# Optimization experiments

Hardware: AMD Instinct MI355X
Metric: run time of the kernel (lower is better)

## Reference

```python
import jax, jax.numpy as jnp
import numpy as np

L, B, T, D, V = 4, 32, 512, 512, 1000


def setup_inputs() -> dict:
    key = jax.random.key(0)
    k0, k1, k2, k3, k4 = jax.random.split(key, 5)
    ids = jax.random.randint(k0, (B, T), 0, V)
    mask = jax.random.randint(k1, (B, T), 0, 2).astype(bool)  # True = valid token
    emb = jax.random.normal(k2, (V, D), dtype=jnp.float32) * 0.1
    W = jax.random.normal(k3, (L, D, 3 * D), dtype=jnp.float32) / np.float32(np.sqrt(D))
    v = jax.random.normal(k4, (L, 2, D), dtype=jnp.float32) * 0.1  # (v_f, v_r) per layer
    b = jnp.zeros((L, 2, D), dtype=jnp.float32)                    # (b_f, b_r) per layer
    return {"ids": ids, "mask": mask, "emb": emb, "W": W, "v": v, "b": b}


def _sru_layer(x, pad, Wl, vf, vr, bf, br):
    # x: [T,B,D] layer input; pad: [T,B,1] bool (True = padded step)
    Tn, Bn, Dn = x.shape
    U = jnp.einsum('tbd,de->tbe', x, Wl).reshape(Tn, Bn, 3, Dn)
    xt, fpre, rpre = U[:, :, 0], U[:, :, 1], U[:, :, 2]

    def step(c, inp):
        xt_t, fp_t, rp_t, x_t, pad_t = inp
        f = jax.nn.sigmoid(fp_t + vf * c + bf)
        r = jax.nn.sigmoid(rp_t + vr * c + br)
        c_new = f * c + (1.0 - f) * xt_t
        h = r * jnp.tanh(c_new) + (1.0 - r) * x_t  # highway (input_size==hidden_size)
        c_out = jnp.where(pad_t, c, c_new)          # padded step: keep state
        h = jnp.where(pad_t, 0.0, h)                # padded step: zero output
        return c_out, h

    c0 = jnp.zeros_like(x[0])  # zero initial hidden state, as in the torch code
    _, h = jax.lax.scan(step, c0, (xt, fpre, rpre, x, pad))
    return h  # [T,B,D]


def reference(ids, mask, emb, W, v, b):
    x = emb[ids]                       # CharEmbedder lookup: [B,T,D]
    x = jnp.transpose(x, (1, 0, 2))    # [T,B,D]  (permute(1,0,2))
    pad = (~mask).T[:, :, None]        # inverted_mask.T -> [T,B,1]
    for l in range(L):
        x = _sru_layer(x, pad, W[l], v[l, 0], v[l, 1], b[l, 0], b[l, 1])
    return jnp.transpose(x, (1, 0, 2))  # back to [B,T,D]
```

## Files before the change

kernel.cpp:

```cpp
#include <hip/hip_runtime.h>
#include <hip/hip_bf16.h>


#define LAYERS 4
#define BB 32
#define TT 512
#define DD 512
#define N3 1536
#define MROWS (TT * BB)
#define WPL ((size_t)DD * N3)
#define SB 32
#define LOG2E 1.4426950408889634f
#define TWOLOG2E 2.8853900817779268f

typedef unsigned short u16;
typedef unsigned int u32;
typedef _Float16 half8 __attribute__((ext_vector_type(8)));
typedef float f32x4 __attribute__((ext_vector_type(4)));

#define SBAR() asm volatile("s_barrier" ::: "memory")
#define WAITVM(n) asm volatile("s_waitcnt vmcnt(" n ")" ::: "memory")

__device__ __forceinline__ float b2f(u16 u) {
  union { unsigned int i; float f; } x;
  x.i = ((unsigned int)u) << 16;
  return x.f;
}
__device__ __forceinline__ u16 f2h(float f) {
  _Float16 h = (_Float16)f;
  return *(u16*)&h;
}
__device__ __forceinline__ float h2f(u16 u) {
  _Float16 h;
  *(u16*)&h = u;
  return (float)h;
}
__device__ __forceinline__ float rcpf(float x) { return __builtin_amdgcn_rcpf(x); }
__device__ __forceinline__ float exp2f_(float x) { return __builtin_amdgcn_exp2f(x); }

__device__ __forceinline__ void async_ld16(const void* g, void* l) {
  __builtin_amdgcn_global_load_lds(
      (const __attribute__((address_space(1))) void*)g,
      (__attribute__((address_space(3))) void*)l, 16, 0, 0);
}
__device__ __forceinline__ void async_ld4(const void* g, void* l) {
  __builtin_amdgcn_global_load_lds(
      (const __attribute__((address_space(1))) void*)g,
      (__attribute__((address_space(3))) void*)l, 4, 0, 0);
}

__global__ void detect_kernel(const u16* __restrict__ emb_u,
                              const int* __restrict__ mask_i,
                              const int* __restrict__ ids_i,
                              int* __restrict__ flags) {
  __shared__ int cnt[3];
  __shared__ int zc;
  int tid = threadIdx.x;
  if (tid < 3) cnt[tid] = 0;
  if (tid == 0) zc = 0;
  __syncthreads();
  int bad = 0, zero_even = 0;
  for (int i = tid; i < 8192; i += 256) {
    u16 u = emb_u[i];
    unsigned e = (u >> 7) & 0xFF;
    if (e >= 0x8F) bad++;
    if ((i & 1) == 0 && u == 0) zero_even++;
  }
  if (bad) atomicAdd(&cnt[0], bad);
  if (zero_even) atomicAdd(&zc, zero_even);
  if (tid < 64) {
    unsigned vv = (unsigned)mask_i[tid];
    if (vv > 1u) atomicAdd(&cnt[1], 1);
  }
  if (tid < 256) {
    if (ids_i[2 * tid + 1] == 0) atomicAdd(&cnt[2], 1);
  }
  __syncthreads();
  if (tid == 0) {
    flags[0] = (cnt[0] > 64 || zc > 3000) ? 1 : 0;
    flags[1] = (cnt[1] > 0) ? 1 : 0;
    flags[2] = (cnt[2] >= 192) ? 1 : 0;
  }
}

__global__ __launch_bounds__(256)
void wprep_kernel(const void* __restrict__ W, u16* __restrict__ W16,
                  const int* __restrict__ flags) {
  __shared__ float tileW[32][33];
  int l = blockIdx.z;
  int k0 = blockIdx.x * 32;
  int n0 = blockIdx.y * 32;
  int tx = threadIdx.x & 31;
  int ty = threadIdx.x >> 5;
  int ff = flags[0];
  const float* Wf = (const float*)W + (size_t)l * WPL;
  const u16* Wb = (const u16*)W + (size_t)l * WPL;
  for (int kk = ty; kk < 32; kk += 8) {
    size_t off = (size_t)(k0 + kk) * N3 + n0 + tx;
    tileW[kk][tx] = ff ? Wf[off] : b2f(Wb[off]);
  }
  __syncthreads();
  u16* outP = W16 + (size_t)l * WPL;
  for (int nn = ty; nn < 32; nn += 8) {
    float x = tileW[tx][nn];
    outP[(size_t)(n0 + nn) * DD + k0 + tx] = f2h(x);
  }
}

__global__ void embed_kernel(const int* __restrict__ ids,
                             const void* __restrict__ emb,
                             u16* __restrict__ X16,
                             const int* __restrict__ flags) {
  int i = blockIdx.x * 256 + threadIdx.x;
  int d = i & (DD - 1);
  int tb = i >> 9;
  int b = tb & (BB - 1);
  int t = tb >> 5;
  int ii = b * TT + t;
  int id = flags[2] ? ids[2 * ii] : ids[ii];
  float val = flags[0] ? ((const float*)emb)[id * DD + d]
                       : b2f(((const u16*)emb)[id * DD + d]);
  X16[i] = f2h(val);
}

__global__ __launch_bounds__(512, 2)
void gemm_kernel(const u16* __restrict__ X16, const u16* __restrict__ W16l,
                 const void* __restrict__ bvec, int layer,
                 const int* __restrict__ flags,
                 u16* __restrict__ U16, int row_base, int chunkM, int nblk) {
  __shared__ u16 lds[2][2][2][8192];
  const int tid = threadIdx.x;
  const int lane = tid & 63, wave = tid >> 6;
  const int wm = wave >> 2, wn = wave & 3;
  const int m16 = lane & 15, quad = lane >> 4;

  const int orig = blockIdx.x;
  const int wg = (orig & 7) * (nblk >> 3) + (orig >> 3);
  const int mt = wg / 6, nt = wg - mt * 6;

  const int arow0 = row_base + mt * 256;
  const int bcol0 = nt * 256;

  const int srow = lane >> 2;
  const int sq = (lane & 3) ^ ((lane >> 3) & 3);
  const u16* pa = X16 + (size_t)(arow0 + wave * 32 + srow) * DD + sq * 8;
  const u16* pb = W16l + (size_t)(bcol0 + wave * 32 + srow) * DD + sq * 8;
  const int ldsblk = wave * 2 * 512;

  auto stage = [&](int s) {
    const int ts = s >> 2, hi = s & 3;
    const int mat = hi & 1, kk = hi >> 1, db = ts & 1;
    const u16* src = (mat ? pb : pa) + ts * 64 + kk * 32;
    u16* dst = &lds[db][mat][kk][ldsblk];
    async_ld16(src, dst);
    async_ld16(src + (size_t)16 * DD, dst + 512);
  };

  f32x4 acc[8][4];
#pragma unroll
  for (int mi = 0; mi < 8; ++mi)
#pragma unroll
    for (int ni = 0; ni < 4; ++ni)
#pragma unroll
      for (int r = 0; r < 4; ++r) acc[mi][ni][r] = 0.f;

#pragma unroll
  for (int s = 0; s < 6; ++s) stage(s);
  WAITVM("8");
  SBAR();

  const int loff = m16 * 32 + (quad ^ ((m16 >> 1) & 3)) * 8;
  half8 bf[4];

  for (int t = 0; t < 8; ++t) {
    const int db = t & 1;
#pragma unroll
    for (int p = 0; p < 4; ++p) {
      const int kk = p >> 1;
      const int mh = (p == 1 || p == 2) ? 1 : 0;
      half8 af[4];
      const u16* Ab = &lds[db][0][kk][(wm * 8 + mh * 4) * 512 + loff];
#pragma unroll
      for (int i = 0; i < 4; ++i) af[i] = *(const half8*)(Ab + i * 512);
      if (p == 0 || p == 2) {
        const u16* Bb = &lds[db][1][kk][wn * 4 * 512 + loff];
#pragma unroll
        for (int i = 0; i < 4; ++i) bf[i] = *(const half8*)(Bb + i * 512);
      }
      const int s = t * 4 + p + 6;
      if (s < 32) stage(s);
      SBAR();
      __builtin_amdgcn_s_setprio(1);
#pragma unroll
      for (int mi = 0; mi < 4; ++mi)
#pragma unroll
        for (int ni = 0; ni < 4; ++ni)
          acc[mh * 4 + mi][ni] = __builtin_amdgcn_mfma_f32_16x16x32_f16(
              af[mi], bf[ni], acc[mh * 4 + mi][ni], 0, 0, 0);
      __builtin_amdgcn_s_setprio(0);
      if (p == 1) {
        WAITVM("4");
      } else if (p == 3) {
        if (t == 6) WAITVM("0");
        else WAITVM("8");
      }
      SBAR();
    }
  }

  const int ff = flags[0];
  const int pl = nt >> 1;
  const int dd0 = (nt & 1) * 256;
  u16* up = U16 + (size_t)pl * chunkM * 512;
  const int r0 = mt * 256 + wm * 128 + quad * 4;
  const int c0 = dd0 + wn * 64 + m16;
  if (pl == 0) {
#pragma unroll
    for (int mi = 0; mi < 8; ++mi)
#pragma unroll
      for (int reg = 0; reg < 4; ++reg) {
        size_t rb = (size_t)(r0 + mi * 16 + reg) * 512 + c0;
#pragma unroll
        for (int ni = 0; ni < 4; ++ni)
          up[rb + ni * 16] = f2h(acc[mi][ni][reg]);
      }
  } else {
    float bias[4];
#pragma unroll
    for (int ni = 0; ni < 4; ++ni) {
      size_t bo = (size_t)layer * 2 * DD + (size_t)(pl - 1) * DD + c0 + ni * 16;
      bias[ni] = ff ? ((const float*)bvec)[bo] : b2f(((const u16*)bvec)[bo]);
    }
#pragma unroll
    for (int mi = 0; mi < 8; ++mi)
#pragma unroll
      for (int reg = 0; reg < 4; ++reg) {
        size_t rb = (size_t)(r0 + mi * 16 + reg) * 512 + c0;
#pragma unroll
        for (int ni = 0; ni < 4; ++ni)
          up[rb + ni * 16] = f2h(-(acc[mi][ni][reg] + bias[ni]) * LOG2E);
      }
  }
}

template <int EMIT>
__global__ __launch_bounds__(448, 1)
void scan_kernel(const u16* __restrict__ U16, float* __restrict__ X,
                 u16* __restrict__ X16,
                 const void* __restrict__ mask_p, const void* __restrict__ vbase,
                 int layer, const int* __restrict__ flags,
                 float* __restrict__ carry, int t0, int nt, int chunkM) {
  __shared__ u16 bufA[2][2][SB][64];
  __shared__ u16 bufB[3][2][SB][64];
  __shared__ float ring[2][2][SB][64];
  __shared__ int msk[TT];
  const int tid = threadIdx.x;
  const int wave = tid >> 6, lane = tid & 63;
  const int idx0 = blockIdx.x * 64;
  const int b = idx0 >> 9;
  const int d0 = idx0 & 511;
  const int ff = flags[0], fm = flags[1];

  const int* mi_ = (const int*)mask_p + b * TT;
  const unsigned char* mb_ = (const unsigned char*)mask_p + b * TT;
  for (int i = tid; i < nt; i += 448) msk[i] = fm ? (int)mb_[t0 + i] : mi_[t0 + i];

  float vfs = 0.f, vrs = 0.f, c = 0.f;
  {
    int d = d0 + lane;
    size_t voff = (size_t)layer * 2 * DD;
    if (wave == 0) {
      float vf = ff ? ((const float*)vbase)[voff + d]
                    : b2f(((const u16*)vbase)[voff + d]);
      vfs = -vf * LOG2E;
      c = (t0 == 0) ? 0.f : carry[idx0 + lane];
    } else if (wave >= 1 && wave <= 4) {
      float vr = ff ? ((const float*)vbase)[voff + DD + d]
                    : b2f(((const u16*)vbase)[voff + DD + d]);
      vrs = -vr * LOG2E;
    }
  }

  const int nbuf = nt / SB;

  auto ld_pair = [&](const u16* rowS, const u16* rowS1, void* ldst) {
    const u32* a0 = (const u32*)rowS;
    const u32* a1 = (const u32*)rowS1;
    const u32* ga = (lane < 32) ? (a0 + lane) : (a1 + (lane - 32));
    async_ld4(ga, ldst);
  };

  auto produceA = [&](int k) {
    int ph = k & 1, tl = k * SB;
    const u16* p0 = U16 + ((size_t)tl * BB + b) * 512 + d0;
    const u16* p1 = p0 + (size_t)chunkM * 512;
#pragma unroll
    for (int s = 0; s < SB; s += 2)
      ld_pair(p0 + (size_t)s * BB * 512, p0 + (size_t)(s + 1) * BB * 512,
              &bufA[ph][0][s][0]);
#pragma unroll
    for (int s = 0; s < SB; s += 2)
      ld_pair(p1 + (size_t)s * BB * 512, p1 + (size_t)(s + 1) * BB * 512,
              &bufA[ph][1][s][0]);
  };
  auto produceB = [&](int k) {
    int ph = k % 3, tl = k * SB;
    const u16* p2 = U16 + 2 * (size_t)chunkM * 512 + ((size_t)tl * BB + b) * 512 + d0;
    const u16* xb = X16 + ((size_t)(t0 + tl) * BB + b) * DD + d0;
#pragma unroll
    for (int s = 0; s < SB; s += 2)
      ld_pair(p2 + (size_t)s * BB * 512, p2 + (size_t)(s + 1) * BB * 512,
              &bufB[ph][0][s][0]);
#pragma unroll
    for (int s = 0; s < SB; s += 2)
      ld_pair(xb + (size_t)s * BB * DD, xb + (size_t)(s + 1) * BB * DD,
              &bufB[ph][1][s][0]);
  };

  float* Xp = X + (size_t)b * TT * DD + d0 + lane;

  auto hphase = [&](int j, int hw) {
    int phc = j & 1, phb = j % 3;
    int sbase = hw * (SB / 4);
#pragma unroll
    for (int si = 0; si < SB / 4; ++si) {
      int s = sbase + si;
      float cprev = ring[phc][0][s][lane];
      float cn = ring[phc][1][s][lane];
      float rps = h2f(bufB[phb][0][s][lane]);
      float xin = h2f(bufB[phb][1][s][lane]);
      int m = msk[j * SB + s];
      float tr = exp2f_(fmaf(vrs, cprev, rps));
      float r = rcpf(1.f + tr);
      float e2 = exp2f_(cn * TWOLOG2E);
      float th = fmaf(-2.f, rcpf(e2 + 1.f), 1.f);
      float h = fmaf(r, th - xin, xin);
      float hout = (m == 0) ? 0.f : h;
      int tg = t0 + j * SB + s;
      if (EMIT)
        X16[((size_t)tg * BB + b) * DD + d0 + lane] = f2h(hout);
      else
        Xp[(size_t)tg * DD] = hout;
    }
  };

  if (wave == 5) produceA(0);
  if (wave == 6) produceB(0);

  for (int k = 0; k < nbuf; ++k) {
    __syncthreads();
    if (wave == 5) {
      if (k + 1 < nbuf) produceA(k + 1);
    } else if (wave == 6) {
      if (k + 1 < nbuf) produceB(k + 1);
    } else if (wave == 0) {
      int ph = k & 1;
#pragma unroll 8
      for (int s = 0; s < SB; ++s) {
        float xt = h2f(bufA[ph][0][s][lane]);
        float fps = h2f(bufA[ph][1][s][lane]);
        float t = exp2f_(fmaf(vfs, c, fps));
        float f = rcpf(1.f + t);
        float cn = fmaf(f, c - xt, xt);
        ring[ph][0][s][lane] = c;
        ring[ph][1][s][lane] = cn;
        c = (msk[k * SB + s] == 0) ? c : cn;
      }
    } else {
      if (k > 0) hphase(k - 1, wave - 1);
    }
  }
  __syncthreads();
  if (wave >= 1 && wave <= 4) hphase(nbuf - 1, wave - 1);
  if (wave == 0) carry[idx0 + lane] = c;
}

__global__ void sentinel_kernel(float* out) { out[threadIdx.x] = 12345.f; }

extern "C" void kernel_launch(void* const* d_in, const int* in_sizes, int n_in,
                              void* d_out, int out_size, void* d_ws, size_t ws_size,
                              hipStream_t stream) {
  const int* ids = (const int*)d_in[0];
  const void* mask = d_in[1];
  const void* emb = d_in[2];
  const void* W = d_in[3];
  const void* v = d_in[4];
  const void* bp = d_in[5];

  char* ws = (char*)d_ws;
  int* flags = (int*)ws;
  float* carry = (float*)(ws + 4096);
  const size_t offX16 = 69632;
  const size_t offW16 = offX16 + (size_t)MROWS * DD * 2;
  const size_t offU = offW16 + (size_t)LAYERS * WPL * 2;
  const size_t perT = (size_t)BB * N3 * 2;

  const int cand[4] = {512, 256, 128, 64};
  int chunkT = 0;
  for (int i = 0; i < 4; ++i) {
    if (ws_size >= offU + (size_t)cand[i] * perT) { chunkT = cand[i]; break; }
  }
  if (!chunkT) {
    sentinel_kernel<<<1, 256, 0, stream>>>((float*)d_out);
    return;
  }
  const int chunkM = chunkT * BB;

  u16* X16 = (u16*)(ws + offX16);
  u16* W16 = (u16*)(ws + offW16);
  u16* U16 = (u16*)(ws + offU);
  float* X = (float*)d_out;

  detect_kernel<<<1, 256, 0, stream>>>((const u16*)emb, (const int*)mask,
                                       (const int*)ids, flags);
  wprep_kernel<<<dim3(16, 48, 4), 256, 0, stream>>>(W, W16, flags);
  embed_kernel<<<MROWS * DD / 256, 256, 0, stream>>>(ids, emb, X16, flags);

  int nch = TT / chunkT;
  for (int l = 0; l < LAYERS; ++l) {
    const u16* W16l = W16 + (size_t)l * WPL;
    for (int ch = 0; ch < nch; ++ch) {
      int t0 = ch * chunkT;
      int nblk = (chunkM / 256) * 6;
      gemm_kernel<<<nblk, 512, 0, stream>>>(X16, W16l, bp, l, flags, U16,
                                            t0 * BB, chunkM, nblk);
      if (l < LAYERS - 1)
        scan_kernel<1><<<BB * DD / 64, 448, 0, stream>>>(U16, X, X16, mask, v, l,
                                                         flags, carry, t0, chunkT,
                                                         chunkM);
      else
        scan_kernel<0><<<BB * DD / 64, 448, 0, stream>>>(U16, X, X16, mask, v, l,
                                                         flags, carry, t0, chunkT,
                                                         chunkM);
    }
  }
}
```

Measured before the change: 361.2 us.

## Shrink GEMM tile to 256x128 with 4x2 wave layout and deeper prefetch

Changes the projection GEMM block tile from 256x256 to 256x128, with waves arranged 4x2 and each wave computing a 64x64 sub-tile. This halves the accumulator registers and doubles the grid size. The LDS staging is restructured into per-k-half stages with three stages in flight and a single barrier per step. The aim is higher occupancy and better latency hiding, at the cost of more redundant A-tile loads across blocks.

```diff
diff --git a/kernel.cpp b/kernel.cpp
--- a/kernel.cpp
+++ b/kernel.cpp
@@ -128,95 +128,85 @@
                  const void* __restrict__ bvec, int layer,
                  const int* __restrict__ flags,
                  u16* __restrict__ U16, int row_base, int chunkM, int nblk) {
-  __shared__ u16 lds[2][2][2][8192];
+  __shared__ u16 ldsA[2][2][8192];
+  __shared__ u16 ldsB[2][2][4096];
   const int tid = threadIdx.x;
   const int lane = tid & 63, wave = tid >> 6;
-  const int wm = wave >> 2, wn = wave & 3;
+  const int wm = wave >> 1, wn = wave & 1;
   const int m16 = lane & 15, quad = lane >> 4;
 
   const int orig = blockIdx.x;
   const int wg = (orig & 7) * (nblk >> 3) + (orig >> 3);
-  const int mt = wg / 6, nt = wg - mt * 6;
+  const int mt = wg / 12, nt = wg - mt * 12;
 
   const int arow0 = row_base + mt * 256;
-  const int bcol0 = nt * 256;
+  const int bcol0 = nt * 128;
 
   const int srow = lane >> 2;
   const int sq = (lane & 3) ^ ((lane >> 3) & 3);
   const u16* pa = X16 + (size_t)(arow0 + wave * 32 + srow) * DD + sq * 8;
-  const u16* pb = W16l + (size_t)(bcol0 + wave * 32 + srow) * DD + sq * 8;
-  const int ldsblk = wave * 2 * 512;
-
-  auto stage = [&](int s) {
-    const int ts = s >> 2, hi = s & 3;
-    const int mat = hi & 1, kk = hi >> 1, db = ts & 1;
-    const u16* src = (mat ? pb : pa) + ts * 64 + kk * 32;
-    u16* dst = &lds[db][mat][kk][ldsblk];
-    async_ld16(src, dst);
-    async_ld16(src + (size_t)16 * DD, dst + 512);
+  const u16* pb = W16l + (size_t)(bcol0 + wave * 16 + srow) * DD + sq * 8;
+
+  auto stage = [&](int h) {
+    const int ts = h >> 1, kk = h & 1, db = ts & 1;
+    const int kv = ts * 64 + kk * 32;
+    async_ld16(pa + kv, &ldsA[db][kk][(2 * wave) * 512]);
+    async_ld16(pa + kv + (size_t)16 * DD, &ldsA[db][kk][(2 * wave + 1) * 512]);
+    async_ld16(pb + kv, &ldsB[db][kk][wave * 512]);
   };
 
-  f32x4 acc[8][4];
-#pragma unroll
-  for (int mi = 0; mi < 8; ++mi)
+  f32x4 acc[4][4];
+#pragma unroll
+  for (int mi = 0; mi < 4; ++mi)
 #pragma unroll
     for (int ni = 0; ni < 4; ++ni)
 #pragma unroll
       for (int r = 0; r < 4; ++r) acc[mi][ni][r] = 0.f;
 
-#pragma unroll
-  for (int s = 0; s < 6; ++s) stage(s);
-  WAITVM("8");
+  stage(0); stage(1); stage(2);
+  WAITVM("6");
   SBAR();
 
   const int loff = m16 * 32 + (quad ^ ((m16 >> 1) & 3)) * 8;
-  half8 bf[4];
-
+
+#pragma unroll
   for (int t = 0; t < 8; ++t) {
     const int db = t & 1;
 #pragma unroll
-    for (int p = 0; p < 4; ++p) {
-      const int kk = p >> 1;
-      const int mh = (p == 1 || p == 2) ? 1 : 0;
-      half8 af[4];
-      const u16* Ab = &lds[db][0][kk][(wm * 8 + mh * 4) * 512 + loff];
-#pragma unroll
-      for (int i = 0; i < 4; ++i) af[i] = *(const half8*)(Ab + i * 512);
-      if (p == 0 || p == 2) {
-        const u16* Bb = &lds[db][1][kk][wn * 4 * 512 + loff];
-#pragma unroll
-        for (int i = 0; i < 4; ++i) bf[i] = *(const half8*)(Bb + i * 512);
-      }
-      const int s = t * 4 + p + 6;
-      if (s < 32) stage(s);
+    for (int kk = 0; kk < 2; ++kk) {
+      const int g = 2 * t + kk;
+      half8 af[4], bf[4];
+#pragma unroll
+      for (int i = 0; i < 4; ++i)
+        af[i] = *(const half8*)&ldsA[db][kk][(wm * 4 + i) * 512 + loff];
+#pragma unroll
+      for (int i = 0; i < 4; ++i)
+        bf[i] = *(const half8*)&ldsB[db][kk][(wn * 4 + i) * 512 + loff];
+      if (g + 3 < 16) stage(g + 3);
+      __builtin_amdgcn_s_setprio(1);
+#pragma unroll
+      for (int mi = 0; mi < 4; ++mi)
+#pragma unroll
+        for (int ni = 0; ni < 4; ++ni)
+          acc[mi][ni] = __builtin_amdgcn_mfma_f32_16x16x32_f16(
+              af[mi], bf[ni], acc[mi][ni], 0, 0, 0);
+      __builtin_amdgcn_s_setprio(0);
+      if (g <= 12) WAITVM("6");
+      else if (g == 13) WAITVM("3");
+      else if (g == 14) WAITVM("0");
       SBAR();
-      __builtin_amdgcn_s_setprio(1);
-#pragma unroll
-      for (int mi = 0; mi < 4; ++mi)
-#pragma unroll
-        for (int ni = 0; ni < 4; ++ni)
-          acc[mh * 4 + mi][ni] = __builtin_amdgcn_mfma_f32_16x16x32_f16(
-              af[mi], bf[ni], acc[mh * 4 + mi][ni], 0, 0, 0);
-      __builtin_amdgcn_s_setprio(0);
-      if (p == 1) {
-        WAITVM("4");
-      } else if (p == 3) {
-        if (t == 6) WAITVM("0");
-        else WAITVM("8");
-      }
-      SBAR();
     }
   }
 
   const int ff = flags[0];
-  const int pl = nt >> 1;
-  const int dd0 = (nt & 1) * 256;
+  const int pl = nt >> 2;
+  const int dd0 = (nt & 3) * 128;
   u16* up = U16 + (size_t)pl * chunkM * 512;
-  const int r0 = mt * 256 + wm * 128 + quad * 4;
+  const int r0 = mt * 256 + wm * 64 + quad * 4;
   const int c0 = dd0 + wn * 64 + m16;
   if (pl == 0) {
 #pragma unroll
-    for (int mi = 0; mi < 8; ++mi)
+    for (int mi = 0; mi < 4; ++mi)
 #pragma unroll
       for (int reg = 0; reg < 4; ++reg) {
         size_t rb = (size_t)(r0 + mi * 16 + reg) * 512 + c0;
@@ -232,7 +222,7 @@
       bias[ni] = ff ? ((const float*)bvec)[bo] : b2f(((const u16*)bvec)[bo]);
     }
 #pragma unroll
-    for (int mi = 0; mi < 8; ++mi)
+    for (int mi = 0; mi < 4; ++mi)
 #pragma unroll
       for (int reg = 0; reg < 4; ++reg) {
         size_t rb = (size_t)(r0 + mi * 16 + reg) * 512 + c0;
@@ -421,7 +411,7 @@
     const u16* W16l = W16 + (size_t)l * WPL;
     for (int ch = 0; ch < nch; ++ch) {
       int t0 = ch * chunkT;
-      int nblk = (chunkM / 256) * 6;
+      int nblk = (chunkM / 256) * 12;
       gemm_kernel<<<nblk, 512, 0, stream>>>(X16, W16l, bp, l, flags, U16,
                                             t0 * BB, chunkM, nblk);
       if (l < LAYERS - 1)
```

Result: slower. 368.4 us (+2.0%).
